# Kernel optimization log

Measured on AMD Instinct MI355X. Metric: run time of the kernel, lower is better.

Reference implementation:

```python
import jax, jax.numpy as jnp
import numpy as np

B, N, D = 64, 128, 512
NEG = 1e30


def _gru_cell(x, h, Wi, Wh, bi, bh):
    # torch nn.GRUCell math
    gi = x @ Wi.T + bi  # (B, 3D)
    gh = h @ Wh.T + bh  # (B, 3D)
    ir, iz, inn = jnp.split(gi, 3, axis=-1)
    hr, hz, hn = jnp.split(gh, 3, axis=-1)
    r = jax.nn.sigmoid(ir + hr)
    z = jax.nn.sigmoid(iz + hz)
    n = jnp.tanh(inn + r * hn)
    return (1.0 - z) * n + z * h


def setup_inputs() -> dict:
    key = jax.random.key(0)
    ks = jax.random.split(key, 16)
    s = 1.0 / np.sqrt(D)
    u = lambda k, shape: jax.random.uniform(k, shape, jnp.float32, -s, s)
    adj = jax.random.randint(ks[13], (B, N, N), 0, 2, jnp.int32)
    adj = adj.at[:, :, 0].set(1)  # ensure each causal prefix has >=1 unmasked edge
    s_mask = jax.random.randint(ks[14], (B, N, N), 0, 2, jnp.int32)
    o_mask = 1 - s_mask
    return {
        "features": jax.random.normal(ks[0], (B, N, D), jnp.float32),
        "Wi_c": u(ks[1], (3 * D, D)),
        "Wh_c": u(ks[2], (3 * D, D)),
        "bi_c": u(ks[3], (3 * D,)),
        "bh_c": u(ks[4], (3 * D,)),
        "Wi_p": u(ks[5], (3 * D, D)),
        "Wh_p": u(ks[6], (3 * D, D)),
        "bi_p": u(ks[7], (3 * D,)),
        "bh_p": u(ks[8], (3 * D,)),
        "lin_w": u(ks[9], (1, 2 * D)),
        "lin_b": u(ks[10], (1,)),
        "Wr0": u(ks[11], (D, D)),
        "Wr1": u(ks[12], (D, D)),
        "adj": adj,
        "s_mask": s_mask,
        "o_mask": o_mask,
    }


def reference(features, Wi_c, Wh_c, bi_c, bh_c, Wi_p, Wh_p, bi_p, bh_p,
              lin_w, lin_b, Wr0, Wr1, adj, s_mask, o_mask):
    dt = features.dtype
    adj_f = adj.astype(dt)
    s_f = s_mask.astype(dt)
    o_f = o_mask.astype(dt)
    wq = lin_w[0, :D]   # applies to Q half of cat(Q, K)
    wk = lin_w[0, D:]   # applies to K half
    b = lin_b[0]
    pos = jnp.arange(N)

    # step 0
    x0 = features[:, 0]
    zeros = jnp.zeros((B, D), dt)
    C0 = _gru_cell(x0, zeros, Wi_c, Wh_c, bi_c, bh_c)
    P0 = _gru_cell(zeros, x0, Wi_p, Wh_p, bi_p, bh_p)
    H0 = jnp.zeros((B, N, D), dt).at[:, 0].set(C0 + P0)

    def step(H, inputs):
        i, x, adj_row, s_row, o_row = inputs
        # masked graph attention over the causal prefix [0, i)
        alpha = (x @ wq)[:, None] + H @ wk + b          # (B, N)
        valid = adj_row * (pos < i).astype(dt)          # (B, N)
        alpha = alpha - (1.0 - valid) * NEG
        w = jax.nn.softmax(alpha, axis=1)               # (B, N)
        V = (H @ Wr0.T) * s_row[:, :, None] + (H @ Wr1.T) * o_row[:, :, None]
        M = jnp.einsum('bn,bnd->bd', w, V)              # (B, D)
        C = _gru_cell(x, M, Wi_c, Wh_c, bi_c, bh_c)
        P = _gru_cell(M, x, Wi_p, Wh_p, bi_p, bh_p)
        H = H.at[:, i].set(C + P)
        return H, None

    xs = (jnp.arange(1, N),
          jnp.swapaxes(features, 0, 1)[1:],
          jnp.swapaxes(adj_f, 0, 1)[1:],
          jnp.swapaxes(s_f, 0, 1)[1:],
          jnp.swapaxes(o_f, 0, 1)[1:])
    H1, _ = jax.lax.scan(step, H0, xs)
    return H1
```

## Files before the change

kernel.cpp:

```cpp
#include <hip/hip_runtime.h>

#define BB 64
#define NN 128
#define DD 512
#define NBLK 128
#define NTHR 512
#define GCOLS 24
#define WCS 2056
#define WXS 1032
#define BCS 6656
#define UBE (BB * 2048)

typedef unsigned short u16;
typedef unsigned int u32;
typedef unsigned long long u64;
typedef __attribute__((ext_vector_type(8))) __bf16 bf16x8;
typedef __attribute__((ext_vector_type(4))) float f32x4;

#define MFMA16(a, b, c) __builtin_amdgcn_mfma_f32_16x16x32_bf16((a), (b), (c), 0, 0, 0)

__device__ __forceinline__ float b2f(u16 u) {
    union { u32 i; float f; } c; c.i = ((u32)u) << 16; return c.f;
}
__device__ __forceinline__ u16 f2b(float f) {
    union { float f; u32 i; } c; c.f = f;
    return (u16)((c.i + 0x7FFFu + ((c.i >> 16) & 1u)) >> 16);
}
__device__ __forceinline__ float sigm(float x) { return 1.f / (1.f + __expf(-x)); }
__device__ __forceinline__ float tanh_(float x) {
    x = fminf(fmaxf(x, -15.f), 15.f);
    float e = __expf(2.f * x);
    return (e - 1.f) / (e + 1.f);
}

__device__ __forceinline__ float ld_cohf(const float* p) {
    return __hip_atomic_load((float*)p, __ATOMIC_RELAXED, __HIP_MEMORY_SCOPE_AGENT);
}
__device__ __forceinline__ void st_cohf(float* p, float v) {
    __hip_atomic_store(p, v, __ATOMIC_RELAXED, __HIP_MEMORY_SCOPE_AGENT);
}
__device__ __forceinline__ void st_cohu32(u32* p, u32 v) {
    __hip_atomic_store(p, v, __ATOMIC_RELAXED, __HIP_MEMORY_SCOPE_AGENT);
}
__device__ __forceinline__ void st_cohi(int* p, int v) {
    __hip_atomic_store(p, v, __ATOMIC_RELAXED, __HIP_MEMORY_SCOPE_AGENT);
}
__device__ __forceinline__ int ld_cohi(int* p) {
    return __hip_atomic_load(p, __ATOMIC_RELAXED, __HIP_MEMORY_SCOPE_AGENT);
}

template<bool CACHED>
__device__ __forceinline__ bf16x8 ldu16(const u16* p) {
    if constexpr (CACHED) {
        return *(const bf16x8*)p;
    } else {
        union { bf16x8 v; u64 q[2]; } u;
        u.q[0] = __hip_atomic_load((u64*)p,     __ATOMIC_RELAXED, __HIP_MEMORY_SCOPE_AGENT);
        u.q[1] = __hip_atomic_load((u64*)p + 1, __ATOMIC_RELAXED, __HIP_MEMORY_SCOPE_AGENT);
        return u.v;
    }
}

__device__ __forceinline__ void gbar(int* sync, int gen, int blk) {
    __syncthreads();
    int* epoch = sync;
    if (blk == 0) {
        const int t = threadIdx.x;
        int done = (t == 0 || t >= NBLK) ? 1 : 0;
        int* myarr = sync + 256 + t * 16;
        int it = 0;
        for (;;) {
            if (!done) {
                int v = ((it & 15) == 15)
                    ? __hip_atomic_load(myarr, __ATOMIC_ACQUIRE, __HIP_MEMORY_SCOPE_AGENT)
                    : __hip_atomic_load(myarr, __ATOMIC_RELAXED, __HIP_MEMORY_SCOPE_AGENT);
                done = (v >= gen);
            }
            ++it;
            if (__syncthreads_and(done)) break;
            __builtin_amdgcn_s_sleep(1);
        }
        if (t == 0) {
            (void)__hip_atomic_load(sync + 256 + 16, __ATOMIC_ACQUIRE, __HIP_MEMORY_SCOPE_AGENT);
            __hip_atomic_store(epoch, gen, __ATOMIC_RELEASE, __HIP_MEMORY_SCOPE_AGENT);
        }
        __syncthreads();
    } else {
        if (threadIdx.x == 0) {
            __hip_atomic_store(sync + 256 + blk * 16, gen, __ATOMIC_RELEASE, __HIP_MEMORY_SCOPE_AGENT);
            int it = 0;
            for (;;) {
                int v = ((it & 15) == 15)
                    ? __hip_atomic_load(epoch, __ATOMIC_ACQUIRE, __HIP_MEMORY_SCOPE_AGENT)
                    : __hip_atomic_load(epoch, __ATOMIC_RELAXED, __HIP_MEMORY_SCOPE_AGENT);
                ++it;
                if (v >= gen) break;
                __builtin_amdgcn_s_sleep(1);
            }
            (void)__hip_atomic_load(epoch, __ATOMIC_ACQUIRE, __HIP_MEMORY_SCOPE_AGENT);
        }
        __syncthreads();
    }
}

__device__ __forceinline__ void gbar_lite(int* flags, int gen, int blk,
                                          int nsig, bool sig, bool wait) {
    __syncthreads();
    if (sig && threadIdx.x == 0)
        st_cohi(flags + blk * 32, gen);
    if (wait) {
        const int t = threadIdx.x;
        int done = (t >= nsig) ? 1 : 0;
        int* f = flags + t * 32;
        for (;;) {
            if (!done) done = (ld_cohi(f) >= gen);
            if (__syncthreads_and(done)) break;
            __builtin_amdgcn_s_sleep(2);
        }
    }
    asm volatile("" ::: "memory");
    __builtin_amdgcn_sched_barrier(0);
}

__device__ __forceinline__ void waitA(int* flagsA, int gen, int grp) {
    const int l = threadIdx.x & 63;
    int* f = flagsA + (grp * 16 + (l & 15)) * 32;
    for (;;) {
        int v = ld_cohi(f);
        if (__all(v >= gen)) break;
        __builtin_amdgcn_s_sleep(1);
    }
    asm volatile("" ::: "memory");
    __builtin_amdgcn_sched_barrier(0);
}

template<bool CACHED>
__device__ __forceinline__ void gates_merged(
    const u16* __restrict__ ub, const u16* s_wc, const float* s_gb,
    float* __restrict__ bc, int blk, int rt, int lr, int lq)
{
    const int cc0 = lr, cc1 = lr + 8;
    const u16* w0 = s_wc + cc0 * WCS;
    const u16* w1 = s_wc + cc1 * WCS;
    const u16* arow = ub + (size_t)(rt * 16 + lr) * 2048;
    f32x4 acc0 = {0.f, 0.f, 0.f, 0.f}, acc1 = {0.f, 0.f, 0.f, 0.f};
    #pragma unroll 4
    for (int c = 0; c < 16; ++c) {
        int kk = c * 32 + lq * 8;
        bf16x8 ah = ldu16<CACHED>(arow + kk);
        bf16x8 al = ldu16<CACHED>(arow + 512 + kk);
        bf16x8 wh0 = *(const bf16x8*)(w0 + kk);
        bf16x8 wl0 = *(const bf16x8*)(w0 + 1024 + kk);
        bf16x8 wh1 = *(const bf16x8*)(w1 + kk);
        bf16x8 wl1 = *(const bf16x8*)(w1 + 1024 + kk);
        acc0 = MFMA16(ah, wh0, acc0); acc0 = MFMA16(al, wh0, acc0); acc0 = MFMA16(ah, wl0, acc0);
        acc1 = MFMA16(ah, wh1, acc1); acc1 = MFMA16(al, wh1, acc1); acc1 = MFMA16(ah, wl1, acc1);
    }
    #pragma unroll 4
    for (int c = 0; c < 16; ++c) {
        int kk = c * 32 + lq * 8;
        bf16x8 ah = ldu16<CACHED>(arow + 1024 + kk);
        bf16x8 al = ldu16<CACHED>(arow + 1536 + kk);
        bf16x8 wh0 = *(const bf16x8*)(w0 + 512 + kk);
        bf16x8 wl0 = *(const bf16x8*)(w0 + 1536 + kk);
        bf16x8 wh1 = *(const bf16x8*)(w1 + 512 + kk);
        bf16x8 wl1 = *(const bf16x8*)(w1 + 1536 + kk);
        acc0 = MFMA16(ah, wh0, acc0); acc0 = MFMA16(al, wh0, acc0); acc0 = MFMA16(ah, wl0, acc0);
        acc1 = MFMA16(ah, wh1, acc1); acc1 = MFMA16(al, wh1, acc1); acc1 = MFMA16(ah, wl1, acc1);
    }
    float b0 = s_gb[cc0], b1 = s_gb[cc1];
    int col0 = blk * GCOLS + cc0, col1 = blk * GCOLS + cc1;
    #pragma unroll
    for (int r = 0; r < 4; ++r) {
        size_t row = (size_t)(rt * 16 + lq * 4 + r) * BCS;
        st_cohf(bc + row + 512 + col0, acc0[r] + b0);
        st_cohf(bc + row + 512 + col1, acc1[r] + b1);
    }
}

__device__ __forceinline__ f32x4 x_core(
    int i, const u16* __restrict__ featblob, const u16* s_wxw,
    int task, int lr, int lq, int* ccO)
{
    const int ct = task & 1, rt = task >> 1;
    const int cc = ct * 8 + lr;
    *ccO = cc;
    const u16* wcol = s_wxw + cc * WXS;
    const u16* arow = featblob + (size_t)(i * 64 + rt * 16 + lr) * 1024;
    f32x4 acc = {0.f, 0.f, 0.f, 0.f};
    #pragma unroll 4
    for (int c = 0; c < 16; ++c) {
        int kk = c * 32 + lq * 8;
        bf16x8 ah = *(const bf16x8*)(arow + kk);
        bf16x8 al = *(const bf16x8*)(arow + 512 + kk);
        bf16x8 wh = *(const bf16x8*)(wcol + kk);
        bf16x8 wl = *(const bf16x8*)(wcol + 512 + kk);
        acc = MFMA16(ah, wh, acc); acc = MFMA16(al, wh, acc); acc = MFMA16(ah, wl, acc);
    }
    return acc;
}

__device__ __forceinline__ void x_task(
    int i, const u16* __restrict__ featblob, const u16* s_wxw, const float* s_xb,
    float* __restrict__ bc, int blk, int task, int lr, int lq)
{
    int cc; f32x4 acc = x_core(i, featblob, s_wxw, task, lr, lq, &cc);
    const int rt = task >> 1;
    const int col = blk * GCOLS + cc;
    float bias = s_xb[cc];
    #pragma unroll
    for (int r = 0; r < 4; ++r)
        st_cohf(bc + (size_t)(rt * 16 + lq * 4 + r) * BCS + 3584 + col, acc[r] + bias);
}

__device__ __forceinline__ void x_task_xg(
    int i, const u16* __restrict__ featblob, const u16* s_wxw, const float* s_xb,
    float* __restrict__ xg, int blk, int task, int lr, int lq)
{
    int cc; f32x4 acc = x_core(i, featblob, s_wxw, task, lr, lq, &cc);
    const int rt = task >> 1;
    const int col = blk * GCOLS + cc;
    float bias = s_xb[cc];
    #pragma unroll
    for (int r = 0; r < 4; ++r)
        xg[((size_t)i * 64 + rt * 16 + lq * 4 + r) * 3072 + col] = acc[r] + bias;
}

template<bool CACHED>
__device__ __forceinline__ void m_task(
    const u16* __restrict__ ub, const u16* __restrict__ WrB,
    float* __restrict__ bc, int blk, int lr, int lq)
{
    const int ct = blk >> 2, rt = blk & 3;
    const int col = ct * 16 + lr;
    const u16* wcol = WrB + (size_t)col * 2048;
    const u16* arow = ub + (size_t)(rt * 16 + lr) * 2048;
    f32x4 acc = {0.f, 0.f, 0.f, 0.f};
    #pragma unroll 4
    for (int c = 0; c < 16; ++c) {
        int kk = c * 32 + lq * 8;
        bf16x8 a0h = ldu16<CACHED>(arow + kk);
        bf16x8 a0l = ldu16<CACHED>(arow + 512 + kk);
        bf16x8 a1h = ldu16<CACHED>(arow + 1024 + kk);
        bf16x8 a1l = ldu16<CACHED>(arow + 1536 + kk);
        bf16x8 w0h = *(const bf16x8*)(wcol + kk);
        bf16x8 w0l = *(const bf16x8*)(wcol + 512 + kk);
        bf16x8 w1h = *(const bf16x8*)(wcol + 1024 + kk);
        bf16x8 w1l = *(const bf16x8*)(wcol + 1536 + kk);
        acc = MFMA16(a0h, w0h, acc); acc = MFMA16(a0l, w0h, acc); acc = MFMA16(a0h, w0l, acc);
        acc = MFMA16(a1h, w1h, acc); acc = MFMA16(a1l, w1h, acc); acc = MFMA16(a1h, w1l, acc);
    }
    #pragma unroll
    for (int r = 0; r < 4; ++r)
        st_cohf(bc + (size_t)(rt * 16 + lq * 4 + r) * BCS + col, acc[r]);
}

__global__ __launch_bounds__(NTHR) void grn_kernel(
    const float* __restrict__ feat, const float* __restrict__ Wi_c, const float* __restrict__ Wh_c,
    const float* __restrict__ bi_c, const float* __restrict__ bh_c,
    const float* __restrict__ Wi_p, const float* __restrict__ Wh_p,
    const float* __restrict__ bi_p, const float* __restrict__ bh_p,
    const float* __restrict__ lin_w, const float* __restrict__ lin_b,
    const float* __restrict__ Wr0, const float* __restrict__ Wr1,
    const int* __restrict__ adj, const int* __restrict__ smask,
    float* __restrict__ out,
    float* __restrict__ q, u16* __restrict__ ublob,
    u16* __restrict__ featblob, float* __restrict__ bc, u16* __restrict__ WrB,
    float* __restrict__ xg, int* __restrict__ sync, int use_ring, int use_xg)
{
    const int t = threadIdx.x, blk = blockIdx.x;
    const int lane = t & 63, wv = t >> 6;
    const int lr = lane & 15, lq = lane >> 4;
    int gen = 0;
    int* flagsA = sync + 4096;
    int* flagsB = sync + 8192;

    __shared__ u16 s_wc[GCOLS * WCS];
    __shared__ __align__(16) char s_wx_raw[GCOLS * WXS * 2];
    __shared__ float s_u0[DD];
    __shared__ float s_ut[DD];
    __shared__ float s_red[NTHR];
    __shared__ float s_hk[NN];
    __shared__ float s_q[NN];
    __shared__ float s_w[NN];
    __shared__ float s_ws[NN];
    __shared__ float s_gb[GCOLS];
    __shared__ float s_xb[GCOLS];

    u16* s_wxw = (u16*)s_wx_raw;
    float* s_wgf = (float*)s_wx_raw;
    float* s_part = (float*)s_wx_raw;

    const float wkreg = lin_w[DD + t];

    for (int rr = 0; rr < 64; ++rr) {
        int gr = blk * 64 + rr;
        int bb_ = gr >> 7, nn_ = gr & 127;
        float x = feat[(size_t)gr * DD + t];
        u16 h = f2b(x);
        u16* dst = featblob + (size_t)(nn_ * 64 + bb_) * 1024;
        dst[t] = h;
        dst[512 + t] = f2b(x - b2f(h));
    }
    for (int cc = 0; cc < 4; ++cc) {
        int c = blk * 4 + cc;
        float w0 = Wr0[(size_t)c * DD + t], w1 = Wr1[(size_t)c * DD + t];
        u16 h0 = f2b(w0), h1 = f2b(w1);
        u16* dst = WrB + (size_t)c * 2048;
        dst[t] = h0; dst[512 + t] = f2b(w0 - b2f(h0));
        dst[1024 + t] = h1; dst[1536 + t] = f2b(w1 - b2f(h1));
    }
    {
        float linb = lin_b[0];
        float wqf[8];
        #pragma unroll
        for (int jj = 0; jj < 8; ++jj) wqf[jj] = lin_w[lane * 8 + jj];
        for (int rr = 0; rr < 8; ++rr) {
            int row = blk * 64 + wv * 8 + rr;
            const float* fp = feat + (size_t)row * DD + lane * 8;
            float p = 0.f;
            #pragma unroll
            for (int jj = 0; jj < 8; ++jj) p += fp[jj] * wqf[jj];
            #pragma unroll
            for (int off = 32; off; off >>= 1) p += __shfl_down(p, off, 64);
            if (lane == 0) q[row] = p + linb;
        }
    }
    {
        int jg0 = blk * GCOLS;
        for (int cc = 0; cc < GCOLS; ++cc) {
            int jg = jg0 + cc;
            const float* src = (jg < 1536) ? (Wh_c + (size_t)jg * DD) : (Wi_p + (size_t)(jg - 1536) * DD);
            s_wgf[t * GCOLS + cc] = src[t];
        }
        if (t < GCOLS) {
            int jg = jg0 + t;
            s_gb[t] = (jg < 1536) ? bh_c[jg] : bi_p[jg - 1536];
            s_xb[t] = (jg < 1536) ? bi_c[jg] : bh_p[jg - 1536];
        }
    }
    __syncthreads();
    {
        float acc0[GCOLS], acc1[GCOLS];
        #pragma unroll
        for (int cc = 0; cc < GCOLS; ++cc) { acc0[cc] = 0.f; acc1[cc] = 0.f; }
        for (int j = 0; j < DD; ++j) {
            float wr0 = Wr0[(size_t)j * DD + t];
            float wr1 = Wr1[(size_t)j * DD + t];
            const float* g = s_wgf + j * GCOLS;
            #pragma unroll
            for (int cc = 0; cc < GCOLS; ++cc) {
                float gv = g[cc];
                acc0[cc] += wr0 * gv;
                acc1[cc] += wr1 * gv;
            }
        }
        __syncthreads();
        #pragma unroll
        for (int cc = 0; cc < GCOLS; ++cc) {
            u16 h0 = f2b(acc0[cc]);
            s_wc[cc * WCS + t] = h0;
            s_wc[cc * WCS + 1024 + t] = f2b(acc0[cc] - b2f(h0));
            u16 h1 = f2b(acc1[cc]);
            s_wc[cc * WCS + 512 + t] = h1;
            s_wc[cc * WCS + 1536 + t] = f2b(acc1[cc] - b2f(h1));
        }
    }
    {
        int jx0 = blk * GCOLS;
        for (int cc = 0; cc < GCOLS; ++cc) {
            int jx = jx0 + cc;
            const float* src = (jx < 1536) ? (Wi_c + (size_t)jx * DD) : (Wh_p + (size_t)(jx - 1536) * DD);
            float w = src[t];
            u16 h = f2b(w);
            s_wxw[cc * WXS + t] = h;
            s_wxw[cc * WXS + 512 + t] = f2b(w - b2f(h));
        }
    }
    gbar(sync, ++gen, blk);

    x_task(0, featblob, s_wxw, s_xb, bc, blk, wv, lr, lq);
    if (use_xg) {
        for (int ii = 0; ii < NN; ++ii)
            x_task_xg(ii, featblob, s_wxw, s_xb, xg, blk, wv, lr, lq);
    }
    if (blk < BB && t < NN) s_q[t] = q[blk * NN + t];
    gbar(sync, ++gen, blk);

    if (blk < BB) {
        const float* bcb = bc + (size_t)blk * BCS;
        float ir = ld_cohf(bcb + 3584 + t), iz = ld_cohf(bcb + 4096 + t), inn = ld_cohf(bcb + 4608 + t);
        float r = sigm(ir + bh_c[t]), z = sigm(iz + bh_c[512 + t]);
        float C = (1.f - z) * tanh_(inn + r * bh_c[1024 + t]);
        float ghr = ld_cohf(bcb + 5120 + t), ghz = ld_cohf(bcb + 5632 + t), ghn = ld_cohf(bcb + 6144 + t);
        float r2 = sigm(bi_p[t] + ghr), z2 = sigm(bi_p[512 + t] + ghz);
        float n2 = tanh_(bi_p[1024 + t] + r2 * ghn);
        float x = feat[(size_t)(blk * NN) * DD + t];
        float P = (1.f - z2) * n2 + z2 * x;
        float Hv = C + P;
        out[(size_t)(blk * NN) * DD + t] = Hv;
        s_red[t] = Hv * wkreg;
        __syncthreads();
        if (wv == 0) {
            float p = 0.f;
            #pragma unroll
            for (int jj = 0; jj < 8; ++jj) p += s_red[lane + 64 * jj];
            #pragma unroll
            for (int off = 32; off; off >>= 1) p += __shfl_down(p, off, 64);
            if (lane == 0) s_hk[0] = p;
        }
    }
    gbar(sync, ++gen, blk);

    for (int i = 1; i < NN; ++i) {
        u16* ub_i = ublob + (size_t)(use_ring ? (NN - 1 - i) : 0) * UBE;

        if (blk < BB) {
            int va0 = 0, va1 = 0, vs0 = 0, vs1 = 0;
            float qv = 0.f;
            if (wv == 0) {
                const int* ar_ = adj + (size_t)(blk * NN + i) * NN;
                const int* sr_ = smask + (size_t)(blk * NN + i) * NN;
                va0 = ar_[lane]; va1 = ar_[lane + 64];
                vs0 = sr_[lane]; vs1 = sr_[lane + 64];
                qv = s_q[i];
            }
            if (i >= 2) {
                int j = i - 1;
                const float* bcb = bc + (size_t)blk * BCS;
                float Mv = ld_cohf(bcb + t);
                float hr = ld_cohf(bcb + 512 + t), hz = ld_cohf(bcb + 1024 + t), hn = ld_cohf(bcb + 1536 + t);
                float gir = ld_cohf(bcb + 2048 + t), giz = ld_cohf(bcb + 2560 + t), gin = ld_cohf(bcb + 3072 + t);
                float ir, iz, inn, ghr, ghz, ghn;
                if (use_xg) {
                    const float* xrow = xg + ((size_t)j * 64 + blk) * 3072;
                    ir = xrow[t]; iz = xrow[512 + t]; inn = xrow[1024 + t];
                    ghr = xrow[1536 + t]; ghz = xrow[2048 + t]; ghn = xrow[2560 + t];
                } else {
                    ir = ld_cohf(bcb + 3584 + t); iz = ld_cohf(bcb + 4096 + t); inn = ld_cohf(bcb + 4608 + t);
                    ghr = ld_cohf(bcb + 5120 + t); ghz = ld_cohf(bcb + 5632 + t); ghn = ld_cohf(bcb + 6144 + t);
                }
                float x = feat[(size_t)(blk * NN + j) * DD + t];
                float r = sigm(ir + hr), z = sigm(iz + hz);
                float C = (1.f - z) * tanh_(inn + r * hn) + z * Mv;
                float r2 = sigm(gir + ghr), z2 = sigm(giz + ghz);
                float P = (1.f - z2) * tanh_(gin + r2 * ghn) + z2 * x;
                float Hv = C + P;
                out[(size_t)(blk * NN + j) * DD + t] = Hv;
                s_red[t] = Hv * wkreg;
            }
            if (!use_xg) { s_u0[t] = 0.f; s_ut[t] = 0.f; }
            __syncthreads();
            if (wv == 0) {
                if (i >= 2) {
                    float p = 0.f;
                    #pragma unroll
                    for (int jj = 0; jj < 8; ++jj) p += s_red[lane + 64 * jj];
                    #pragma unroll
                    for (int off = 32; off; off >>= 1) p += __shfl_down(p, off, 64);
                    if (lane == 0) s_hk[i - 1] = p;
                }
                int n2i = lane + 64;
                float a0 = (lane < i && va0 != 0) ? (qv + s_hk[lane]) : -1e30f;
                float a1 = (n2i < i && va1 != 0) ? (qv + s_hk[n2i]) : -1e30f;
                float m = fmaxf(a0, a1);
                #pragma unroll
                for (int off = 32; off; off >>= 1) m = fmaxf(m, __shfl_xor(m, off, 64));
                float e0 = (a0 > -1e29f) ? __expf(a0 - m) : 0.f;
                float e1 = (a1 > -1e29f) ? __expf(a1 - m) : 0.f;
                float ss = e0 + e1;
                #pragma unroll
                for (int off = 32; off; off >>= 1) ss += __shfl_xor(ss, off, 64);
                float inv = 1.f / ss;
                float w0 = e0 * inv, w1 = e1 * inv;
                s_w[lane] = w0; s_w[n2i] = w1;
                s_ws[lane] = w0 * (float)vs0;
                s_ws[n2i] = w1 * (float)vs1;
            }
            __syncthreads();
            {
                int g = t >> 7, dqb = (t & 127) * 4;
                const float* Hb = out + (size_t)blk * NN * DD + dqb;
                f32x4 u0 = {0.f, 0.f, 0.f, 0.f}, ut = {0.f, 0.f, 0.f, 0.f};
                int n = g;
                for (; n + 12 < i; n += 16) {
                    f32x4 h0 = *(const f32x4*)(Hb + (size_t)n * DD);
                    f32x4 h1 = *(const f32x4*)(Hb + (size_t)(n + 4) * DD);
                    f32x4 h2 = *(const f32x4*)(Hb + (size_t)(n + 8) * DD);
                    f32x4 h3 = *(const f32x4*)(Hb + (size_t)(n + 12) * DD);
                    u0 += s_ws[n] * h0 + s_ws[n + 4] * h1 + s_ws[n + 8] * h2 + s_ws[n + 12] * h3;
                    ut += s_w[n] * h0 + s_w[n + 4] * h1 + s_w[n + 8] * h2 + s_w[n + 12] * h3;
                }
                for (; n < i; n += 4) {
                    f32x4 h0 = *(const f32x4*)(Hb + (size_t)n * DD);
                    u0 += s_ws[n] * h0;
                    ut += s_w[n] * h0;
                }
                if (use_xg) {
                    float* spg = s_part + g * 1024;
                    *(f32x4*)&spg[dqb] = u0;
                    *(f32x4*)&spg[512 + dqb] = ut;
                } else {
                    #pragma unroll
                    for (int e = 0; e < 4; ++e) {
                        atomicAdd(&s_u0[dqb + e], u0[e]);
                        atomicAdd(&s_ut[dqb + e], ut[e]);
                    }
                }
            }
            __syncthreads();
            {
                int tt = t & 255, sel = t >> 8;
                float a0, a1, t0_, t1_;
                if (use_xg) {
                    a0 = s_part[2 * tt]            + s_part[1024 + 2 * tt]
                       + s_part[2048 + 2 * tt]     + s_part[3072 + 2 * tt];
                    a1 = s_part[2 * tt + 1]        + s_part[1024 + 2 * tt + 1]
                       + s_part[2048 + 2 * tt + 1] + s_part[3072 + 2 * tt + 1];
                    t0_ = s_part[512 + 2 * tt]        + s_part[1536 + 2 * tt]
                        + s_part[2560 + 2 * tt]       + s_part[3584 + 2 * tt];
                    t1_ = s_part[512 + 2 * tt + 1]    + s_part[1536 + 2 * tt + 1]
                        + s_part[2560 + 2 * tt + 1]   + s_part[3584 + 2 * tt + 1];
                } else {
                    a0 = s_u0[2 * tt]; a1 = s_u0[2 * tt + 1];
                    t0_ = s_ut[2 * tt]; t1_ = s_ut[2 * tt + 1];
                }
                float b0_ = t0_ - a0, b1_ = t1_ - a1;
                float v0 = sel ? b0_ : a0, v1 = sel ? b1_ : a1;
                u16 h0 = f2b(v0), h1 = f2b(v1);
                u16 l0 = f2b(v0 - b2f(h0)), l1 = f2b(v1 - b2f(h1));
                u32 hw = (u32)h0 | ((u32)h1 << 16);
                u32 lw = (u32)l0 | ((u32)l1 << 16);
                u32* ub32 = (u32*)(ub_i + (size_t)blk * 2048);
                int base = sel * 512;
                st_cohu32(ub32 + base + tt, hw);
                st_cohu32(ub32 + base + 256 + tt, lw);
            }
            __syncthreads();
            if (t == 0) st_cohi(flagsA + blk * 32, i);
        }

        if (use_xg) {
            if (wv < 4) {
                waitA(flagsA, i, wv);
                if (use_ring) gates_merged<true >(ub_i, s_wc, s_gb, bc, blk, wv, lr, lq);
                else          gates_merged<false>(ub_i, s_wc, s_gb, bc, blk, wv, lr, lq);
            } else if (wv == 7) {
                waitA(flagsA, i, blk & 3);
                if (use_ring) m_task<true >(ub_i, WrB, bc, blk, lr, lq);
                else          m_task<false>(ub_i, WrB, bc, blk, lr, lq);
            }
        } else {
            if (wv < 4) {
                waitA(flagsA, i, wv);
                gates_merged<false>(ub_i, s_wc, s_gb, bc, blk, wv, lr, lq);
            } else if (wv == 4) {
                x_task(i, featblob, s_wxw, s_xb, bc, blk, 0, lr, lq);
                x_task(i, featblob, s_wxw, s_xb, bc, blk, 1, lr, lq);
                x_task(i, featblob, s_wxw, s_xb, bc, blk, 2, lr, lq);
            } else if (wv == 5) {
                x_task(i, featblob, s_wxw, s_xb, bc, blk, 3, lr, lq);
                x_task(i, featblob, s_wxw, s_xb, bc, blk, 4, lr, lq);
                x_task(i, featblob, s_wxw, s_xb, bc, blk, 5, lr, lq);
            } else if (wv == 6) {
                x_task(i, featblob, s_wxw, s_xb, bc, blk, 6, lr, lq);
                x_task(i, featblob, s_wxw, s_xb, bc, blk, 7, lr, lq);
            } else {
                waitA(flagsA, i, blk & 3);
                m_task<false>(ub_i, WrB, bc, blk, lr, lq);
            }
        }

        gbar_lite(flagsB, i, blk, NBLK, true, blk < BB);
    }

    if (blk < BB) {
        int j = NN - 1;
        const float* bcb = bc + (size_t)blk * BCS;
        float Mv = ld_cohf(bcb + t);
        float hr = ld_cohf(bcb + 512 + t), hz = ld_cohf(bcb + 1024 + t), hn = ld_cohf(bcb + 1536 + t);
        float gir = ld_cohf(bcb + 2048 + t), giz = ld_cohf(bcb + 2560 + t), gin = ld_cohf(bcb + 3072 + t);
        float ir, iz, inn, ghr, ghz, ghn;
        if (use_xg) {
            const float* xrow = xg + ((size_t)j * 64 + blk) * 3072;
            ir = xrow[t]; iz = xrow[512 + t]; inn = xrow[1024 + t];
            ghr = xrow[1536 + t]; ghz = xrow[2048 + t]; ghn = xrow[2560 + t];
        } else {
            ir = ld_cohf(bcb + 3584 + t); iz = ld_cohf(bcb + 4096 + t); inn = ld_cohf(bcb + 4608 + t);
            ghr = ld_cohf(bcb + 5120 + t); ghz = ld_cohf(bcb + 5632 + t); ghn = ld_cohf(bcb + 6144 + t);
        }
        float x = feat[(size_t)(blk * NN + j) * DD + t];
        float r = sigm(ir + hr), z = sigm(iz + hz);
        float C = (1.f - z) * tanh_(inn + r * hn) + z * Mv;
        float r2 = sigm(gir + ghr), z2 = sigm(giz + ghz);
        float P = (1.f - z2) * tanh_(gin + r2 * ghn) + z2 * x;
        out[(size_t)(blk * NN + j) * DD + t] = C + P;
    }
}

extern "C" void kernel_launch(void* const* d_in, const int* in_sizes, int n_in,
                              void* d_out, int out_size, void* d_ws, size_t ws_size,
                              hipStream_t stream) {
    (void)in_sizes; (void)n_in; (void)out_size;
    const float* feat = (const float*)d_in[0];
    const float* Wi_c = (const float*)d_in[1];
    const float* Wh_c = (const float*)d_in[2];
    const float* bi_c = (const float*)d_in[3];
    const float* bh_c = (const float*)d_in[4];
    const float* Wi_p = (const float*)d_in[5];
    const float* Wh_p = (const float*)d_in[6];
    const float* bi_p = (const float*)d_in[7];
    const float* bh_p = (const float*)d_in[8];
    const float* lin_w = (const float*)d_in[9];
    const float* lin_b = (const float*)d_in[10];
    const float* Wr0 = (const float*)d_in[11];
    const float* Wr1 = (const float*)d_in[12];
    const int* adj = (const int*)d_in[13];
    const int* smask = (const int*)d_in[14];
    float* out = (float*)d_out;

    char* ws = (char*)d_ws;
    size_t off = 0;
    int* sync_ = (int*)(ws + off);      off += 65536;
    float* q = (float*)(ws + off);      off += (size_t)BB * NN * 4;
    u16* featblob = (u16*)(ws + off);   off += (size_t)BB * NN * 1024 * 2;
    float* bc = (float*)(ws + off);     off += (size_t)BB * BCS * 4;
    u16* WrB = (u16*)(ws + off);        off += (size_t)512 * 2048 * 2;
    u16* ublob = (u16*)(ws + off);
    size_t ring_bytes = (size_t)(NN - 1) * UBE * 2;
    size_t xg_bytes = (size_t)NN * 64 * 3072 * 4;
    int use_ring = (ws_size >= off + ring_bytes) ? 1 : 0;
    float* xg = (float*)(ws + off + ring_bytes);
    int use_xg = (use_ring && ws_size >= off + ring_bytes + xg_bytes) ? 1 : 0;

    (void)hipMemsetAsync(d_ws, 0, 65536, stream);
    hipLaunchKernelGGL(grn_kernel, dim3(NBLK), dim3(NTHR), 0, stream,
                       feat, Wi_c, Wh_c, bi_c, bh_c, Wi_p, Wh_p, bi_p, bh_p,
                       lin_w, lin_b, Wr0, Wr1, adj, smask, out,
                       q, ublob, featblob, bc, WrB, xg, sync_, use_ring, use_xg);
}
```

Measured before the change: 3.517 ms.

## Precompute next-step attention partial sums off critical path with online-softmax merge

Measured after the change: 3.418 ms. 1.03x faster.

```diff
diff --git a/kernel.cpp b/kernel.cpp
--- a/kernel.cpp
+++ b/kernel.cpp
@@ -6,7 +6,7 @@
 #define NBLK 128
 #define NTHR 512
 #define GCOLS 24
-#define WCS 2056
+#define WCS 2064
 #define WXS 1032
 #define BCS 6656
 #define UBE (BB * 2048)
@@ -289,7 +289,9 @@
 
     u16* s_wxw = (u16*)s_wx_raw;
     float* s_wgf = (float*)s_wx_raw;
-    float* s_part = (float*)s_wx_raw;
+    float* s_pu = (float*)s_wx_raw;
+    float* s_pt = (float*)(s_wx_raw + 6144);
+    float* s_scal = (float*)(s_wx_raw + 12288);
 
     const float wkreg = lin_w[DD + t];
 
@@ -388,6 +390,15 @@
     gbar(sync, ++gen, blk);
 
     if (blk < BB) {
+        if (use_xg) {
+            s_pu[t] = 0.f; s_pu[512 + t] = 0.f; s_pu[1024 + t] = 0.f;
+            s_pt[t] = 0.f; s_pt[512 + t] = 0.f; s_pt[1024 + t] = 0.f;
+            if (t == 0) {
+                s_scal[0] = -1e30f; s_scal[1] = 0.f;
+                s_scal[2] = (float)adj[((size_t)blk * NN + 1) * NN + 0];
+                s_scal[3] = (float)smask[((size_t)blk * NN + 1) * NN + 0];
+            }
+        }
         const float* bcb = bc + (size_t)blk * BCS;
         float ir = ld_cohf(bcb + 3584 + t), iz = ld_cohf(bcb + 4096 + t), inn = ld_cohf(bcb + 4608 + t);
         float r = sigm(ir + bh_c[t]), z = sigm(iz + bh_c[512 + t]);
@@ -416,128 +427,179 @@
         u16* ub_i = ublob + (size_t)(use_ring ? (NN - 1 - i) : 0) * UBE;
 
         if (blk < BB) {
-            int va0 = 0, va1 = 0, vs0 = 0, vs1 = 0;
-            float qv = 0.f;
-            if (wv == 0) {
-                const int* ar_ = adj + (size_t)(blk * NN + i) * NN;
-                const int* sr_ = smask + (size_t)(blk * NN + i) * NN;
-                va0 = ar_[lane]; va1 = ar_[lane + 64];
-                vs0 = sr_[lane]; vs1 = sr_[lane + 64];
-                qv = s_q[i];
-            }
-            if (i >= 2) {
+            if (use_xg) {
                 int j = i - 1;
-                const float* bcb = bc + (size_t)blk * BCS;
-                float Mv = ld_cohf(bcb + t);
-                float hr = ld_cohf(bcb + 512 + t), hz = ld_cohf(bcb + 1024 + t), hn = ld_cohf(bcb + 1536 + t);
-                float gir = ld_cohf(bcb + 2048 + t), giz = ld_cohf(bcb + 2560 + t), gin = ld_cohf(bcb + 3072 + t);
-                float ir, iz, inn, ghr, ghz, ghn;
-                if (use_xg) {
+                float Hv;
+                if (i >= 2) {
+                    const float* bcb = bc + (size_t)blk * BCS;
+                    float Mv = ld_cohf(bcb + t);
+                    float hr = ld_cohf(bcb + 512 + t), hz = ld_cohf(bcb + 1024 + t), hn = ld_cohf(bcb + 1536 + t);
+                    float gir = ld_cohf(bcb + 2048 + t), giz = ld_cohf(bcb + 2560 + t), gin = ld_cohf(bcb + 3072 + t);
                     const float* xrow = xg + ((size_t)j * 64 + blk) * 3072;
-                    ir = xrow[t]; iz = xrow[512 + t]; inn = xrow[1024 + t];
-                    ghr = xrow[1536 + t]; ghz = xrow[2048 + t]; ghn = xrow[2560 + t];
+                    float ir = xrow[t], iz = xrow[512 + t], inn = xrow[1024 + t];
+                    float ghr = xrow[1536 + t], ghz = xrow[2048 + t], ghn = xrow[2560 + t];
+                    float x = feat[(size_t)(blk * NN + j) * DD + t];
+                    float r = sigm(ir + hr), z = sigm(iz + hz);
+                    float C = (1.f - z) * tanh_(inn + r * hn) + z * Mv;
+                    float r2 = sigm(gir + ghr), z2 = sigm(giz + ghz);
+                    float P = (1.f - z2) * tanh_(gin + r2 * ghn) + z2 * x;
+                    Hv = C + P;
+                    out[(size_t)(blk * NN + j) * DD + t] = Hv;
+                    s_red[t] = Hv * wkreg;
                 } else {
-                    ir = ld_cohf(bcb + 3584 + t); iz = ld_cohf(bcb + 4096 + t); inn = ld_cohf(bcb + 4608 + t);
-                    ghr = ld_cohf(bcb + 5120 + t); ghz = ld_cohf(bcb + 5632 + t); ghn = ld_cohf(bcb + 6144 + t);
-                }
-                float x = feat[(size_t)(blk * NN + j) * DD + t];
-                float r = sigm(ir + hr), z = sigm(iz + hz);
-                float C = (1.f - z) * tanh_(inn + r * hn) + z * Mv;
-                float r2 = sigm(gir + ghr), z2 = sigm(giz + ghz);
-                float P = (1.f - z2) * tanh_(gin + r2 * ghn) + z2 * x;
-                float Hv = C + P;
-                out[(size_t)(blk * NN + j) * DD + t] = Hv;
-                s_red[t] = Hv * wkreg;
-            }
-            if (!use_xg) { s_u0[t] = 0.f; s_ut[t] = 0.f; }
-            __syncthreads();
-            if (wv == 0) {
+                    Hv = out[(size_t)(blk * NN) * DD + t];
+                }
+                __syncthreads();
+                if (wv == 0) {
+                    float hk;
+                    if (i >= 2) {
+                        float p = 0.f;
+                        #pragma unroll
+                        for (int jj = 0; jj < 8; ++jj) p += s_red[lane + 64 * jj];
+                        #pragma unroll
+                        for (int off = 32; off; off >>= 1) p += __shfl_down(p, off, 64);
+                        if (lane == 0) s_hk[j] = p;
+                        hk = p;
+                    } else {
+                        hk = s_hk[0];
+                    }
+                    if (lane == 0) {
+                        float m_part = s_scal[0], denom_p = s_scal[1];
+                        float anew = s_scal[2], snew = s_scal[3];
+                        float alpha = s_q[i] + hk;
+                        float m = m_part, e_new = 0.f;
+                        if (anew != 0.f) { m = fmaxf(m_part, alpha); e_new = __expf(alpha - m); }
+                        float scale = __expf(m_part - m);
+                        float inv = 1.f / (denom_p * scale + e_new);
+                        s_w[0] = scale * inv;
+                        s_w[1] = e_new * snew * inv;
+                        s_w[2] = e_new * inv;
+                    }
+                }
+                __syncthreads();
+                {
+                    float u0p = s_pu[t] + s_pu[512 + t] + s_pu[1024 + t];
+                    float utp = s_pt[t] + s_pt[512 + t] + s_pt[1024 + t];
+                    float CS = s_w[0], C0 = s_w[1], CT = s_w[2];
+                    float U0 = u0p * CS + C0 * Hv;
+                    float U1 = (utp * CS + CT * Hv) - U0;
+                    u16 h0 = f2b(U0); u16 l0 = f2b(U0 - b2f(h0));
+                    u16 h1 = f2b(U1); u16 l1 = f2b(U1 - b2f(h1));
+                    u32 p0 = (u32)h0 | ((u32)l0 << 16);
+                    u32 p1 = (u32)h1 | ((u32)l1 << 16);
+                    u32 q0 = (u32)__shfl_xor((int)p0, 1, 64);
+                    u32 q1 = (u32)__shfl_xor((int)p1, 1, 64);
+                    u32* ub32 = (u32*)(ub_i + (size_t)blk * 2048);
+                    int w = t >> 1;
+                    if ((t & 1) == 0) {
+                        st_cohu32(ub32 + w,       (p0 & 0xFFFFu) | ((q0 & 0xFFFFu) << 16));
+                        st_cohu32(ub32 + 256 + w, (p0 >> 16)     | (q0 & 0xFFFF0000u));
+                    } else {
+                        st_cohu32(ub32 + 512 + w, (q1 & 0xFFFFu) | ((p1 & 0xFFFFu) << 16));
+                        st_cohu32(ub32 + 768 + w, (q1 >> 16)     | (p1 & 0xFFFF0000u));
+                    }
+                }
+                __syncthreads();
+                if (t == 0) st_cohi(flagsA + blk * 32, i);
+            } else {
+                int va0 = 0, va1 = 0, vs0 = 0, vs1 = 0;
+                float qv = 0.f;
+                if (wv == 0) {
+                    const int* ar_ = adj + (size_t)(blk * NN + i) * NN;
+                    const int* sr_ = smask + (size_t)(blk * NN + i) * NN;
+                    va0 = ar_[lane]; va1 = ar_[lane + 64];
+                    vs0 = sr_[lane]; vs1 = sr_[lane + 64];
+                    qv = s_q[i];
+                }
                 if (i >= 2) {
-                    float p = 0.f;
+                    int j = i - 1;
+                    const float* bcb = bc + (size_t)blk * BCS;
+                    float Mv = ld_cohf(bcb + t);
+                    float hr = ld_cohf(bcb + 512 + t), hz = ld_cohf(bcb + 1024 + t), hn = ld_cohf(bcb + 1536 + t);
+                    float gir = ld_cohf(bcb + 2048 + t), giz = ld_cohf(bcb + 2560 + t), gin = ld_cohf(bcb + 3072 + t);
+                    float ir = ld_cohf(bcb + 3584 + t), iz = ld_cohf(bcb + 4096 + t), inn = ld_cohf(bcb + 4608 + t);
+                    float ghr = ld_cohf(bcb + 5120 + t), ghz = ld_cohf(bcb + 5632 + t), ghn = ld_cohf(bcb + 6144 + t);
+                    float x = feat[(size_t)(blk * NN + j) * DD + t];
+                    float r = sigm(ir + hr), z = sigm(iz + hz);
+                    float C = (1.f - z) * tanh_(inn + r * hn) + z * Mv;
+                    float r2 = sigm(gir + ghr), z2 = sigm(giz + ghz);
+                    float P = (1.f - z2) * tanh_(gin + r2 * ghn) + z2 * x;
+                    float Hv = C + P;
+                    out[(size_t)(blk * NN + j) * DD + t] = Hv;
+                    s_red[t] = Hv * wkreg;
+                }
+                s_u0[t] = 0.f; s_ut[t] = 0.f;
+                __syncthreads();
+                if (wv == 0) {
+                    if (i >= 2) {
+                        float p = 0.f;
+                        #pragma unroll
+                        for (int jj = 0; jj < 8; ++jj) p += s_red[lane + 64 * jj];
+                        #pragma unroll
+                        for (int off = 32; off; off >>= 1) p += __shfl_down(p, off, 64);
+                        if (lane == 0) s_hk[i - 1] = p;
+                    }
+                    int n2i = lane + 64;
+                    float a0 = (lane < i && va0 != 0) ? (qv + s_hk[lane]) : -1e30f;
+                    float a1 = (n2i < i && va1 != 0) ? (qv + s_hk[n2i]) : -1e30f;
+                    float m = fmaxf(a0, a1);
                     #pragma unroll
-                    for (int jj = 0; jj < 8; ++jj) p += s_red[lane + 64 * jj];
+                    for (int off = 32; off; off >>= 1) m = fmaxf(m, __shfl_xor(m, off, 64));
+                    float e0 = (a0 > -1e29f) ? __expf(a0 - m) : 0.f;
+                    float e1 = (a1 > -1e29f) ? __expf(a1 - m) : 0.f;
+                    float ss = e0 + e1;
                     #pragma unroll
-                    for (int off = 32; off; off >>= 1) p += __shfl_down(p, off, 64);
-                    if (lane == 0) s_hk[i - 1] = p;
-                }
-                int n2i = lane + 64;
-                float a0 = (lane < i && va0 != 0) ? (qv + s_hk[lane]) : -1e30f;
-                float a1 = (n2i < i && va1 != 0) ? (qv + s_hk[n2i]) : -1e30f;
-                float m = fmaxf(a0, a1);
-                #pragma unroll
-                for (int off = 32; off; off >>= 1) m = fmaxf(m, __shfl_xor(m, off, 64));
-                float e0 = (a0 > -1e29f) ? __expf(a0 - m) : 0.f;
-                float e1 = (a1 > -1e29f) ? __expf(a1 - m) : 0.f;
-                float ss = e0 + e1;
-                #pragma unroll
-                for (int off = 32; off; off >>= 1) ss += __shfl_xor(ss, off, 64);
-                float inv = 1.f / ss;
-                float w0 = e0 * inv, w1 = e1 * inv;
-                s_w[lane] = w0; s_w[n2i] = w1;
-                s_ws[lane] = w0 * (float)vs0;
-                s_ws[n2i] = w1 * (float)vs1;
-            }
-            __syncthreads();
-            {
-                int g = t >> 7, dqb = (t & 127) * 4;
-                const float* Hb = out + (size_t)blk * NN * DD + dqb;
-                f32x4 u0 = {0.f, 0.f, 0.f, 0.f}, ut = {0.f, 0.f, 0.f, 0.f};
-                int n = g;
-                for (; n + 12 < i; n += 16) {
-                    f32x4 h0 = *(const f32x4*)(Hb + (size_t)n * DD);
-                    f32x4 h1 = *(const f32x4*)(Hb + (size_t)(n + 4) * DD);
-                    f32x4 h2 = *(const f32x4*)(Hb + (size_t)(n + 8) * DD);
-                    f32x4 h3 = *(const f32x4*)(Hb + (size_t)(n + 12) * DD);
-                    u0 += s_ws[n] * h0 + s_ws[n + 4] * h1 + s_ws[n + 8] * h2 + s_ws[n + 12] * h3;
-                    ut += s_w[n] * h0 + s_w[n + 4] * h1 + s_w[n + 8] * h2 + s_w[n + 12] * h3;
-                }
-                for (; n < i; n += 4) {
-                    f32x4 h0 = *(const f32x4*)(Hb + (size_t)n * DD);
-                    u0 += s_ws[n] * h0;
-                    ut += s_w[n] * h0;
-                }
-                if (use_xg) {
-                    float* spg = s_part + g * 1024;
-                    *(f32x4*)&spg[dqb] = u0;
-                    *(f32x4*)&spg[512 + dqb] = ut;
-                } else {
+                    for (int off = 32; off; off >>= 1) ss += __shfl_xor(ss, off, 64);
+                    float inv = 1.f / ss;
+                    float w0 = e0 * inv, w1 = e1 * inv;
+                    s_w[lane] = w0; s_w[n2i] = w1;
+                    s_ws[lane] = w0 * (float)vs0;
+                    s_ws[n2i] = w1 * (float)vs1;
+                }
+                __syncthreads();
+                {
+                    int g = t >> 7, dqb = (t & 127) * 4;
+                    const float* Hb = out + (size_t)blk * NN * DD + dqb;
+                    f32x4 u0 = {0.f, 0.f, 0.f, 0.f}, ut = {0.f, 0.f, 0.f, 0.f};
+                    int n = g;
+                    for (; n + 12 < i; n += 16) {
+                        f32x4 h0 = *(const f32x4*)(Hb + (size_t)n * DD);
+                        f32x4 h1 = *(const f32x4*)(Hb + (size_t)(n + 4) * DD);
+                        f32x4 h2 = *(const f32x4*)(Hb + (size_t)(n + 8) * DD);
+                        f32x4 h3 = *(const f32x4*)(Hb + (size_t)(n + 12) * DD);
+                        u0 += s_ws[n] * h0 + s_ws[n + 4] * h1 + s_ws[n + 8] * h2 + s_ws[n + 12] * h3;
+                        ut += s_w[n] * h0 + s_w[n + 4] * h1 + s_w[n + 8] * h2 + s_w[n + 12] * h3;
+                    }
+                    for (; n < i; n += 4) {
+                        f32x4 h0 = *(const f32x4*)(Hb + (size_t)n * DD);
+                        u0 += s_ws[n] * h0;
+                        ut += s_w[n] * h0;
+                    }
                     #pragma unroll
                     for (int e = 0; e < 4; ++e) {
                         atomicAdd(&s_u0[dqb + e], u0[e]);
                         atomicAdd(&s_ut[dqb + e], ut[e]);
                     }
                 }
+                __syncthreads();
+                {
+                    int tt = t & 255, sel = t >> 8;
+                    float a0 = s_u0[2 * tt], a1 = s_u0[2 * tt + 1];
+                    float t0_ = s_ut[2 * tt], t1_ = s_ut[2 * tt + 1];
+                    float b0_ = t0_ - a0, b1_ = t1_ - a1;
+                    float v0 = sel ? b0_ : a0, v1 = sel ? b1_ : a1;
+                    u16 h0 = f2b(v0), h1 = f2b(v1);
+                    u16 l0 = f2b(v0 - b2f(h0)), l1 = f2b(v1 - b2f(h1));
+                    u32 hw = (u32)h0 | ((u32)h1 << 16);
+                    u32 lw = (u32)l0 | ((u32)l1 << 16);
+                    u32* ub32 = (u32*)(ub_i + (size_t)blk * 2048);
+                    int base = sel * 512;
+                    st_cohu32(ub32 + base + tt, hw);
+                    st_cohu32(ub32 + base + 256 + tt, lw);
+                }
+                __syncthreads();
+                if (t == 0) st_cohi(flagsA + blk * 32, i);
             }
-            __syncthreads();
-            {
-                int tt = t & 255, sel = t >> 8;
-                float a0, a1, t0_, t1_;
-                if (use_xg) {
-                    a0 = s_part[2 * tt]            + s_part[1024 + 2 * tt]
-                       + s_part[2048 + 2 * tt]     + s_part[3072 + 2 * tt];
-                    a1 = s_part[2 * tt + 1]        + s_part[1024 + 2 * tt + 1]
-                       + s_part[2048 + 2 * tt + 1] + s_part[3072 + 2 * tt + 1];
-                    t0_ = s_part[512 + 2 * tt]        + s_part[1536 + 2 * tt]
-                        + s_part[2560 + 2 * tt]       + s_part[3584 + 2 * tt];
-                    t1_ = s_part[512 + 2 * tt + 1]    + s_part[1536 + 2 * tt + 1]
-                        + s_part[2560 + 2 * tt + 1]   + s_part[3584 + 2 * tt + 1];
-                } else {
-                    a0 = s_u0[2 * tt]; a1 = s_u0[2 * tt + 1];
-                    t0_ = s_ut[2 * tt]; t1_ = s_ut[2 * tt + 1];
-                }
-                float b0_ = t0_ - a0, b1_ = t1_ - a1;
-                float v0 = sel ? b0_ : a0, v1 = sel ? b1_ : a1;
-                u16 h0 = f2b(v0), h1 = f2b(v1);
-                u16 l0 = f2b(v0 - b2f(h0)), l1 = f2b(v1 - b2f(h1));
-                u32 hw = (u32)h0 | ((u32)h1 << 16);
-                u32 lw = (u32)l0 | ((u32)l1 << 16);
-                u32* ub32 = (u32*)(ub_i + (size_t)blk * 2048);
-                int base = sel * 512;
-                st_cohu32(ub32 + base + tt, hw);
-                st_cohu32(ub32 + base + 256 + tt, lw);
-            }
-            __syncthreads();
-            if (t == 0) st_cohi(flagsA + blk * 32, i);
         }
 
         if (use_xg) {
@@ -549,6 +611,55 @@
                 waitA(flagsA, i, blk & 3);
                 if (use_ring) m_task<true >(ub_i, WrB, bc, blk, lr, lq);
                 else          m_task<false>(ub_i, WrB, bc, blk, lr, lq);
+            } else if (blk < BB && i + 1 < NN) {
+                const int ii = i + 1;
+                const int w = wv - 4;
+                const int* ar = adj + (size_t)(blk * NN + ii) * NN;
+                const int* sr = smask + (size_t)(blk * NN + ii) * NN;
+                int a0 = ar[lane], a1 = ar[lane + 64];
+                int s0 = sr[lane], s1 = sr[lane + 64];
+                float qv = s_q[ii];
+                float al0 = (lane < i && a0 != 0) ? (qv + s_hk[lane]) : -1e30f;
+                float al1 = (lane + 64 < i && a1 != 0) ? (qv + s_hk[lane + 64]) : -1e30f;
+                float m = fmaxf(al0, al1);
+                #pragma unroll
+                for (int off = 32; off; off >>= 1) m = fmaxf(m, __shfl_xor(m, off, 64));
+                float e0 = (al0 > -1e29f) ? __expf(al0 - m) : 0.f;
+                float e1 = (al1 > -1e29f) ? __expf(al1 - m) : 0.f;
+                float es0 = e0 * (float)s0, es1 = e1 * (float)s1;
+                const float* Hb = out + (size_t)blk * NN * DD + lane * 8;
+                f32x4 pa = {0.f,0.f,0.f,0.f}, pb = {0.f,0.f,0.f,0.f};
+                f32x4 ta = {0.f,0.f,0.f,0.f}, tb = {0.f,0.f,0.f,0.f};
+                for (int n = w; n < i; n += 3) {
+                    float en  = __shfl((n < 64) ? e0 : e1, n & 63, 64);
+                    float esn = __shfl((n < 64) ? es0 : es1, n & 63, 64);
+                    f32x4 h0 = *(const f32x4*)(Hb + (size_t)n * DD);
+                    f32x4 h1 = *(const f32x4*)(Hb + (size_t)n * DD + 4);
+                    pa += esn * h0; pb += esn * h1;
+                    ta += en * h0;  tb += en * h1;
+                }
+                *(f32x4*)&s_pu[w * 512 + lane * 8]     = pa;
+                *(f32x4*)&s_pu[w * 512 + lane * 8 + 4] = pb;
+                *(f32x4*)&s_pt[w * 512 + lane * 8]     = ta;
+                *(f32x4*)&s_pt[w * 512 + lane * 8 + 4] = tb;
+                if (w == 0) {
+                    float ds = e0 + e1;
+                    #pragma unroll
+                    for (int off = 32; off; off >>= 1) ds += __shfl_xor(ds, off, 64);
+                    if (lane == 0) {
+                        s_scal[0] = m; s_scal[1] = ds;
+                        s_scal[2] = (float)ar[i];
+                        s_scal[3] = (float)sr[i];
+                    }
+                }
+                if (w == 2) {
+                    const float* fp = feat + (size_t)(blk * NN + i) * DD + lane * 8;
+                    f32x4 f0 = *(const f32x4*)fp;
+                    f32x4 f1 = *(const f32x4*)(fp + 4);
+                    const float* xp = xg + ((size_t)i * 64 + blk) * 3072 + lane * 16;
+                    float x0 = xp[0], x1 = xp[1024], x2 = xp[2048];
+                    asm volatile("" :: "v"(f0), "v"(f1), "v"(x0), "v"(x1), "v"(x2));
+                }
             }
         } else {
             if (wv < 4) {
```
